# Kernel optimization log

Measured on AMD Instinct MI355X. Metric: run time of the kernel, lower is better.

## Reference

```python
import jax, jax.numpy as jnp
import numpy as np

NUM_NODES = 50000
NUM_GRAPHS = 64
HIDDEN = 256
F_IN = 256
NUM_EDGES = 800000


def setup_inputs() -> dict:
    key = jax.random.key(0)
    ks = jax.random.split(key, 8)
    x = jax.random.normal(ks[0], (NUM_NODES, F_IN), dtype=jnp.float32)
    edge_index = jax.random.randint(ks[1], (2, NUM_EDGES), 0, NUM_NODES, dtype=jnp.int64)
    batch = jnp.sort(jax.random.randint(ks[2], (NUM_NODES,), 0, NUM_GRAPHS, dtype=jnp.int64))
    # Glorot-ish init for weights, zeros for biases (as PyG GCNConv / Linear defaults)
    s1 = 1.0 / np.sqrt(F_IN)
    s2 = 1.0 / np.sqrt(HIDDEN)
    W1 = jax.random.uniform(ks[3], (F_IN, HIDDEN), jnp.float32, -s1, s1)
    b1 = jnp.zeros((HIDDEN,), jnp.float32)
    W2 = jax.random.uniform(ks[4], (HIDDEN, HIDDEN), jnp.float32, -s2, s2)
    b2 = jnp.zeros((HIDDEN,), jnp.float32)
    W_out = jax.random.uniform(ks[5], (HIDDEN, 1), jnp.float32, -s2, s2)
    b_out = jnp.zeros((1,), jnp.float32)
    return {"x": x, "edge_index": edge_index, "batch": batch,
            "W1": W1, "b1": b1, "W2": W2, "b2": b2,
            "W_out": W_out, "b_out": b_out}


def gcn_conv(x, W, b, src, dst, num_nodes):
    """GCNConv with added self-loops and symmetric D^{-1/2} A D^{-1/2} norm."""
    # degrees over edges incl. self-loops (src/dst already include them)
    deg = jax.ops.segment_sum(jnp.ones_like(src, dtype=x.dtype), dst,
                              num_segments=num_nodes)
    dinv = jax.lax.rsqrt(jnp.maximum(deg, 1e-12))
    norm = dinv[src] * dinv[dst]                       # [E+N]
    h = x @ W                                           # [N, H] dense GEMM
    msg = h[src] * norm[:, None]                        # gather + scale
    out = jax.ops.segment_sum(msg, dst, num_segments=num_nodes)  # scatter-add
    return out + b


def reference(x, edge_index, batch, W1, b1, W2, b2, W_out, b_out):
    n = x.shape[0]
    loops = jnp.arange(n, dtype=edge_index.dtype)
    src = jnp.concatenate([edge_index[0], loops])
    dst = jnp.concatenate([edge_index[1], loops])
    h = jax.nn.relu(gcn_conv(x, W1, b1, src, dst, n))
    h = jax.nn.relu(gcn_conv(h, W2, b2, src, dst, n))
    pooled = jax.ops.segment_sum(h, batch, num_segments=NUM_GRAPHS)  # [G, H]
    return pooled @ W_out + b_out
```

## Files before the change

kernel.cpp:

```cpp
#include <hip/hip_runtime.h>
#include <hip/hip_fp16.h>

#define N_NODES 50000
#define NFEAT   256
#define NGRAPH  64
#define NEDGE   800000
#define NBLK_SCAN 196

typedef __attribute__((ext_vector_type(8))) _Float16 half8;
typedef __attribute__((ext_vector_type(2))) _Float16 h2v;
typedef __attribute__((ext_vector_type(4))) float f32x4;
struct alignas(8) US4 { unsigned short x, y, z, w; };

static __device__ __forceinline__ float h2f(unsigned short u) {
    return __half2float(__ushort_as_half(u));
}
static __device__ __forceinline__ unsigned short f2h(float f) {
    return __half_as_ushort(__float2half(f));
}

__global__ void k_count(const int* __restrict__ dst, int* __restrict__ cnt) {
    int e = blockIdx.x * 256 + threadIdx.x;
    if (e < NEDGE) atomicAdd(&cnt[dst[e]], 1);
}

__global__ __launch_bounds__(256) void k_scan1(const int* __restrict__ cnt,
                                               int* __restrict__ row_start,
                                               int* __restrict__ bsum) {
    const int t = threadIdx.x, i = blockIdx.x * 256 + t;
    const int lane = t & 63, w = t >> 6;
    const int c = (i < N_NODES) ? cnt[i] : 0;
    int incl = c;
#pragma unroll
    for (int off = 1; off < 64; off <<= 1) {
        int u = __shfl_up(incl, off, 64);
        if (lane >= off) incl += u;
    }
    __shared__ int wtot[4];
    if (lane == 63) wtot[w] = incl;
    __syncthreads();
    int wbase = 0;
#pragma unroll
    for (int k = 0; k < 4; ++k) wbase += (k < w) ? wtot[k] : 0;
    if (i < N_NODES) row_start[i] = wbase + incl - c;
    if (t == 255) bsum[blockIdx.x] = wbase + incl;
}

__global__ __launch_bounds__(256) void k_scan2(int* __restrict__ bsum) {
    const int t = threadIdx.x, lane = t & 63, w = t >> 6;
    const int c = (t < NBLK_SCAN) ? bsum[t] : 0;
    int incl = c;
#pragma unroll
    for (int off = 1; off < 64; off <<= 1) {
        int u = __shfl_up(incl, off, 64);
        if (lane >= off) incl += u;
    }
    __shared__ int wtot[4];
    if (lane == 63) wtot[w] = incl;
    __syncthreads();
    int wbase = 0;
#pragma unroll
    for (int k = 0; k < 4; ++k) wbase += (k < w) ? wtot[k] : 0;
    if (t < NBLK_SCAN) bsum[t] = wbase + incl - c;
}

__global__ void k_scan3(int* __restrict__ row_start, const int* __restrict__ bsum,
                        int* __restrict__ cnt_cursor, float* __restrict__ dinv) {
    const int i = blockIdx.x * 256 + threadIdx.x;
    if (i >= N_NODES) return;
    const int c = cnt_cursor[i];
    const int start = row_start[i] + bsum[blockIdx.x];
    row_start[i] = start;
    cnt_cursor[i] = start;
    dinv[i] = rsqrtf((float)c + 1.0f);
    if (i == 0) row_start[N_NODES] = NEDGE;
}

__global__ void k_place(const int* __restrict__ src, const int* __restrict__ dst,
                        int* __restrict__ cursor, const float* __restrict__ dinv,
                        unsigned int* __restrict__ csr) {
    int e = blockIdx.x * 256 + threadIdx.x;
    if (e < NEDGE) {
        int s = src[e], d = dst[e];
        float norm = dinv[s] * dinv[d];
        int pos = atomicAdd(&cursor[d], 1);
        csr[pos] = ((unsigned int)f2h(norm) << 16) | (unsigned int)s;
    }
}

__global__ void k_prep_w(const float* __restrict__ W1, const float* __restrict__ W2,
                         unsigned short* __restrict__ w1t, unsigned short* __restrict__ w2t) {
    const int l = blockIdx.x >> 8;
    const int idx = (blockIdx.x & 255) * 256 + threadIdx.x;
    const int n = idx >> 8, k = idx & 255;
    const float* W = l ? W2 : W1;
    unsigned short* wt = l ? w2t : w1t;
    wt[n * 256 + k] = f2h(W[k * 256 + n]);
}

template <bool AF32>
__global__ __launch_bounds__(256) void k_gemm_mfma(const float* __restrict__ Af,
                                                   const unsigned short* __restrict__ Ah,
                                                   const unsigned short* __restrict__ Wt,
                                                   unsigned short* __restrict__ Ch, int M) {
    __shared__ unsigned short lds[32768];
    const int t = threadIdx.x;
    const int half = blockIdx.y;
    const int m0 = blockIdx.x * 128;
    const int w = t >> 6, lane = t & 63;
    const int lr = lane & 15, g = lane >> 4;

    {
        const unsigned short* wbase = Wt + (size_t)half * 128 * 256;
#pragma unroll
        for (int it = 0; it < 16; ++it) {
            const int unit = it * 256 + t;
            const int n = unit >> 5;
            const int rem = unit & 31;
            const int ks = rem >> 2, kg = rem & 3;
            const half8 v = *(const half8*)&wbase[n * 256 + rem * 8];
            const int kgx = kg ^ ((n >> 1) & 3);
            *(half8*)&lds[ks * 4096 + n * 32 + kgx * 8] = v;
        }
    }
    __syncthreads();

    const int rbase = m0 + w * 32;
    unsigned short* Chh = Ch + (size_t)half * (size_t)N_NODES * 128;

    half8 aA[8], aB[8];

#define LOADCHUNK(C, DST)                                                                \
    {                                                                                    \
        const int row = min(rbase + (C) * 16 + lr, M - 1);                               \
        _Pragma("unroll") for (int ks = 0; ks < 8; ++ks) {                               \
            if (AF32) {                                                                  \
                const float* ap = Af + (size_t)row * 256 + ks * 32 + g * 8;              \
                const float4 p0 = *(const float4*)ap;                                    \
                const float4 p1 = *(const float4*)(ap + 4);                              \
                half8 h;                                                                 \
                h[0] = (_Float16)p0.x; h[1] = (_Float16)p0.y;                            \
                h[2] = (_Float16)p0.z; h[3] = (_Float16)p0.w;                            \
                h[4] = (_Float16)p1.x; h[5] = (_Float16)p1.y;                            \
                h[6] = (_Float16)p1.z; h[7] = (_Float16)p1.w;                            \
                DST[ks] = h;                                                             \
            } else {                                                                     \
                DST[ks] = *(const half8*)(Ah + (size_t)(ks >> 2) * (size_t)N_NODES * 128 \
                                          + (size_t)row * 128 + (ks & 3) * 32 + g * 8);  \
            }                                                                            \
        }                                                                                \
    }

#define COMPUTE(C, SRC)                                                                  \
    {                                                                                    \
        f32x4 acc[8] = {};                                                               \
        _Pragma("unroll") for (int ks = 0; ks < 8; ++ks) {                               \
            _Pragma("unroll") for (int ni = 0; ni < 8; ++ni) {                           \
                const int n = ni * 16 + lr;                                              \
                const half8 bf = *(const half8*)&lds[ks * 4096 + n * 32 +                \
                                                     ((g ^ ((n >> 1) & 3)) << 3)];       \
                acc[ni] = __builtin_amdgcn_mfma_f32_16x16x32_f16(SRC[ks], bf,            \
                                                                 acc[ni], 0, 0, 0);      \
            }                                                                            \
        }                                                                                \
        const int r0 = rbase + (C) * 16 + g * 4;                                         \
        _Pragma("unroll") for (int ni = 0; ni < 8; ++ni) {                               \
            const int col = ni * 16 + lr;                                                \
            _Pragma("unroll") for (int r = 0; r < 4; ++r) {                              \
                if (r0 + r < M) Chh[(size_t)(r0 + r) * 128 + col] = f2h(acc[ni][r]);     \
            }                                                                            \
        }                                                                                \
    }

    LOADCHUNK(0, aA)
    LOADCHUNK(1, aB)
    COMPUTE(0, aA)
    COMPUTE(1, aB)

#undef LOADCHUNK
#undef COMPUTE
}

__global__ __launch_bounds__(256) void k_aggregate(const unsigned short* __restrict__ h16,
                                                   const int* __restrict__ row_start,
                                                   const unsigned int* __restrict__ csr,
                                                   const float* __restrict__ dinv,
                                                   const float* __restrict__ bias,
                                                   unsigned short* __restrict__ out,
                                                   const int half) {
    const int node = blockIdx.x * 4 + (threadIdx.x >> 6);
    if (node >= N_NODES) return;
    const int lane = threadIdx.x & 63;
    const int sub = lane >> 4;
    const int fl = lane & 15;
    const unsigned int* hu = (const unsigned int*)(h16 + (size_t)half * N_NODES * 128);

    float acc[8] = {};
    const int s0 = row_start[node], s1 = row_start[node + 1];
    const unsigned int* row = csr + s0;
    const int n = s1 - s0;

#define EDGEPAIR(EA, EB)                                                              \
    {                                                                                 \
        const unsigned int wnp = __builtin_amdgcn_perm(EB, EA, 0x07060302u);          \
        const h2v wn2 = __builtin_bit_cast(h2v, wnp);                                 \
        const uint4 va = *(const uint4*)(hu + (size_t)((EA)&0xffffu) * 64 + fl * 4);  \
        const uint4 vb = *(const uint4*)(hu + (size_t)((EB)&0xffffu) * 64 + fl * 4);  \
        unsigned int plo, phi;                                                        \
        plo = __builtin_amdgcn_perm(vb.x, va.x, 0x05040100u);                         \
        phi = __builtin_amdgcn_perm(vb.x, va.x, 0x07060302u);                         \
        acc[0] = __builtin_amdgcn_fdot2(__builtin_bit_cast(h2v, plo), wn2, acc[0], false); \
        acc[1] = __builtin_amdgcn_fdot2(__builtin_bit_cast(h2v, phi), wn2, acc[1], false); \
        plo = __builtin_amdgcn_perm(vb.y, va.y, 0x05040100u);                         \
        phi = __builtin_amdgcn_perm(vb.y, va.y, 0x07060302u);                         \
        acc[2] = __builtin_amdgcn_fdot2(__builtin_bit_cast(h2v, plo), wn2, acc[2], false); \
        acc[3] = __builtin_amdgcn_fdot2(__builtin_bit_cast(h2v, phi), wn2, acc[3], false); \
        plo = __builtin_amdgcn_perm(vb.z, va.z, 0x05040100u);                         \
        phi = __builtin_amdgcn_perm(vb.z, va.z, 0x07060302u);                         \
        acc[4] = __builtin_amdgcn_fdot2(__builtin_bit_cast(h2v, plo), wn2, acc[4], false); \
        acc[5] = __builtin_amdgcn_fdot2(__builtin_bit_cast(h2v, phi), wn2, acc[5], false); \
        plo = __builtin_amdgcn_perm(vb.w, va.w, 0x05040100u);                         \
        phi = __builtin_amdgcn_perm(vb.w, va.w, 0x07060302u);                         \
        acc[6] = __builtin_amdgcn_fdot2(__builtin_bit_cast(h2v, plo), wn2, acc[6], false); \
        acc[7] = __builtin_amdgcn_fdot2(__builtin_bit_cast(h2v, phi), wn2, acc[7], false); \
    }

    const int nfull = n & ~7;
    int j = 0;
    for (; j < nfull; j += 8) {
        const unsigned int ea = row[j + sub * 2];
        const unsigned int eb = row[j + sub * 2 + 1];
        EDGEPAIR(ea, eb)
    }
    if (j < n) {
        const int ia = j + sub * 2, ib = ia + 1;
        const unsigned int ea = (ia < n) ? row[ia] : 0u;
        const unsigned int eb = (ib < n) ? row[ib] : 0u;
        EDGEPAIR(ea, eb)
    }
#undef EDGEPAIR

#pragma unroll
    for (int i = 0; i < 8; ++i) {
        acc[i] += __shfl_xor(acc[i], 16, 64);
        acc[i] += __shfl_xor(acc[i], 32, 64);
    }

    if (sub == 0) {
        const float dd = dinv[node];
        const float ws = dd * dd;
        const uint4 sh = *(const uint4*)(hu + (size_t)node * 64 + fl * 4);
        const float4 b0 = *(const float4*)(bias + half * 128 + fl * 8);
        const float4 b1 = *(const float4*)(bias + half * 128 + fl * 8 + 4);
        float r[8];
        r[0] = fmaf(h2f((unsigned short)(sh.x & 0xffff)), ws, acc[0]) + b0.x;
        r[1] = fmaf(h2f((unsigned short)(sh.x >> 16)),    ws, acc[1]) + b0.y;
        r[2] = fmaf(h2f((unsigned short)(sh.y & 0xffff)), ws, acc[2]) + b0.z;
        r[3] = fmaf(h2f((unsigned short)(sh.y >> 16)),    ws, acc[3]) + b0.w;
        r[4] = fmaf(h2f((unsigned short)(sh.z & 0xffff)), ws, acc[4]) + b1.x;
        r[5] = fmaf(h2f((unsigned short)(sh.z >> 16)),    ws, acc[5]) + b1.y;
        r[6] = fmaf(h2f((unsigned short)(sh.w & 0xffff)), ws, acc[6]) + b1.z;
        r[7] = fmaf(h2f((unsigned short)(sh.w >> 16)),    ws, acc[7]) + b1.w;
#pragma unroll
        for (int i = 0; i < 8; ++i) r[i] = fmaxf(r[i], 0.f);
        uint4 o;
        o.x = (unsigned int)f2h(r[0]) | ((unsigned int)f2h(r[1]) << 16);
        o.y = (unsigned int)f2h(r[2]) | ((unsigned int)f2h(r[3]) << 16);
        o.z = (unsigned int)f2h(r[4]) | ((unsigned int)f2h(r[5]) << 16);
        o.w = (unsigned int)f2h(r[6]) | ((unsigned int)f2h(r[7]) << 16);
        *(uint4*)((unsigned int*)(out + (size_t)half * N_NODES * 128) +
                  (size_t)node * 64 + fl * 4) = o;
    }
}

__global__ void k_pool(const unsigned short* __restrict__ h2, const int* __restrict__ batch,
                       float* __restrict__ pooled) {
    const int strip = blockIdx.x * 2 + (threadIdx.x >> 7);
    const int tf = threadIdx.x & 127;
    const int f = tf * 2;
    const unsigned short* base = h2 + (size_t)(f >> 7) * N_NODES * 128 + (f & 127);
    const int n0 = strip * 40, n1 = n0 + 40;
    int g = batch[n0];
    float ax = 0.f, ay = 0.f;
    for (int n = n0; n < n1; ++n) {
        const int bg = batch[n];
        if (bg != g) {
            unsafeAtomicAdd(&pooled[g * NFEAT + f], ax);
            unsafeAtomicAdd(&pooled[g * NFEAT + f + 1], ay);
            ax = ay = 0.f;
            g = bg;
        }
        const unsigned int u = *(const unsigned int*)(base + (size_t)n * 128);
        ax += h2f((unsigned short)(u & 0xffff));
        ay += h2f((unsigned short)(u >> 16));
    }
    unsafeAtomicAdd(&pooled[g * NFEAT + f], ax);
    unsafeAtomicAdd(&pooled[g * NFEAT + f + 1], ay);
}

__global__ void k_final(const float* __restrict__ pooled, const float* __restrict__ Wout,
                        const float* __restrict__ bout, float* __restrict__ out) {
    const int g = blockIdx.x, t = threadIdx.x;
    float v = pooled[g * NFEAT + t] * Wout[t];
#pragma unroll
    for (int off = 32; off > 0; off >>= 1) v += __shfl_down(v, off, 64);
    __shared__ float sred[4];
    if ((t & 63) == 0) sred[t >> 6] = v;
    __syncthreads();
    if (t == 0) out[g] = sred[0] + sred[1] + sred[2] + sred[3] + bout[0];
}

extern "C" void kernel_launch(void* const* d_in, const int* in_sizes, int n_in,
                              void* d_out, int out_size, void* d_ws, size_t ws_size,
                              hipStream_t stream) {
    const float* x     = (const float*)d_in[0];
    const int*   ei    = (const int*)d_in[1];
    const int*   batch = (const int*)d_in[2];
    const float* W1    = (const float*)d_in[3];
    const float* b1    = (const float*)d_in[4];
    const float* W2    = (const float*)d_in[5];
    const float* b2    = (const float*)d_in[6];
    const float* Wout  = (const float*)d_in[7];
    const float* bout  = (const float*)d_in[8];
    float* out = (float*)d_out;

    const int* srcp = ei;
    const int* dstp = ei + NEDGE;

    const size_t NE128 = (size_t)N_NODES * 128;
    unsigned short* hA = (unsigned short*)d_ws;
    unsigned short* hB = hA + 2 * NE128;
    float* dinv      = (float*)(hB + 2 * NE128);
    float* pooled    = dinv + N_NODES;
    int*   cnt       = (int*)(pooled + NGRAPH * NFEAT);
    int*   row_start = cnt + N_NODES;
    int*   bsum      = row_start + N_NODES + 3;
    unsigned int* csr = (unsigned int*)(bsum + 256);
    unsigned short* w1t = (unsigned short*)(csr + NEDGE);
    unsigned short* w2t = w1t + 65536;

    const int nblk_edges = (NEDGE + 255) / 256;

    hipMemsetAsync(cnt, 0, N_NODES * sizeof(int), stream);
    k_count<<<nblk_edges, 256, 0, stream>>>(dstp, cnt);
    k_scan1<<<NBLK_SCAN, 256, 0, stream>>>(cnt, row_start, bsum);
    k_scan2<<<1, 256, 0, stream>>>(bsum);
    k_scan3<<<NBLK_SCAN, 256, 0, stream>>>(row_start, bsum, cnt, dinv);
    k_place<<<nblk_edges, 256, 0, stream>>>(srcp, dstp, cnt, dinv, csr);

    k_prep_w<<<512, 256, 0, stream>>>(W1, W2, w1t, w2t);

    const dim3 ggrid(391, 2);
    const int agg_grid = (N_NODES + 3) / 4;

    k_gemm_mfma<true><<<ggrid, 256, 0, stream>>>(x, nullptr, w1t, hA, N_NODES);
    k_aggregate<<<agg_grid, 256, 0, stream>>>(hA, row_start, csr, dinv, b1, hB, 0);
    k_aggregate<<<agg_grid, 256, 0, stream>>>(hA, row_start, csr, dinv, b1, hB, 1);

    k_gemm_mfma<false><<<ggrid, 256, 0, stream>>>(nullptr, hB, w2t, hA, N_NODES);
    k_aggregate<<<agg_grid, 256, 0, stream>>>(hA, row_start, csr, dinv, b2, hB, 0);
    k_aggregate<<<agg_grid, 256, 0, stream>>>(hA, row_start, csr, dinv, b2, hB, 1);

    hipMemsetAsync(pooled, 0, NGRAPH * NFEAT * sizeof(float), stream);
    k_pool<<<625, 256, 0, stream>>>(hB, batch, pooled);
    k_final<<<NGRAPH, 256, 0, stream>>>(pooled, Wout, bout, out);
}
```

Before: 290.2 us.

## Bucket-sort CSR build and fold dinv scaling into GEMM epilogue

Replaces the global-atomic count, three-stage scan and atomic place with a two-level bucket sort: edges are binned into 512-node buckets with LDS histograms, then each bucket builds its CSR rows with LDS atomics. The symmetric norm is factored out: the GEMM epilogue pre-scales rows by dinv[src], and the aggregate multiplies by dinv[dst] once, so the CSR stores only 16-bit source indices. This halves CSR bytes and removes global atomics, but assumes per-bucket edge counts fit in a fixed 16384 window and node ids fit in 16 bits.

```diff
diff --git a/kernel.cpp b/kernel.cpp
--- a/kernel.cpp
+++ b/kernel.cpp
@@ -5,7 +5,8 @@
 #define NFEAT   256
 #define NGRAPH  64
 #define NEDGE   800000
-#define NBLK_SCAN 196
+#define NBUCK   98
+#define BWIN    16384
 
 typedef __attribute__((ext_vector_type(8))) _Float16 half8;
 typedef __attribute__((ext_vector_type(2))) _Float16 h2v;
@@ -19,73 +20,109 @@
     return __half_as_ushort(__float2half(f));
 }
 
-__global__ void k_count(const int* __restrict__ dst, int* __restrict__ cnt) {
-    int e = blockIdx.x * 256 + threadIdx.x;
-    if (e < NEDGE) atomicAdd(&cnt[dst[e]], 1);
-}
-
-__global__ __launch_bounds__(256) void k_scan1(const int* __restrict__ cnt,
+__global__ __launch_bounds__(256) void k_bin(const int* __restrict__ src,
+                                             const int* __restrict__ dst,
+                                             int* __restrict__ bcnt,
+                                             unsigned int* __restrict__ tmp) {
+    __shared__ int hist[NBUCK];
+    __shared__ int base[NBUCK];
+    const int t = threadIdx.x;
+    if (t < NBUCK) hist[t] = 0;
+    __syncthreads();
+    const int e0 = blockIdx.x * 1024 + t * 4;
+    int s[4], d[4], b[4], rk[4];
+#pragma unroll
+    for (int i = 0; i < 4; ++i) {
+        const int e = e0 + i;
+        if (e < NEDGE) {
+            s[i] = src[e];
+            d[i] = dst[e];
+            b[i] = d[i] >> 9;
+            rk[i] = atomicAdd(&hist[b[i]], 1);
+        } else {
+            b[i] = -1;
+        }
+    }
+    __syncthreads();
+    if (t < NBUCK) base[t] = atomicAdd(&bcnt[t], hist[t]);
+    __syncthreads();
+#pragma unroll
+    for (int i = 0; i < 4; ++i) {
+        if (b[i] >= 0)
+            tmp[(size_t)b[i] * BWIN + base[b[i]] + rk[i]] =
+                ((unsigned int)s[i] << 16) | (unsigned int)d[i];
+    }
+}
+
+__global__ void k_bscan(const int* __restrict__ bcnt, int* __restrict__ bbase) {
+    const int l = threadIdx.x;
+    const int i0 = 2 * l, i1 = 2 * l + 1;
+    const int v0 = (i0 < NBUCK) ? bcnt[i0] : 0;
+    const int v1 = (i1 < NBUCK) ? bcnt[i1] : 0;
+    const int ps = v0 + v1;
+    int incl = ps;
+#pragma unroll
+    for (int off = 1; off < 64; off <<= 1) {
+        int u = __shfl_up(incl, off, 64);
+        if (l >= off) incl += u;
+    }
+    const int excl = incl - ps;
+    if (i0 < NBUCK) bbase[i0] = excl;
+    if (i1 < NBUCK) bbase[i1] = excl + v0;
+}
+
+__global__ __launch_bounds__(256) void k_build(const unsigned int* __restrict__ tmp,
+                                               const int* __restrict__ bcnt,
+                                               const int* __restrict__ bbase,
                                                int* __restrict__ row_start,
-                                               int* __restrict__ bsum) {
-    const int t = threadIdx.x, i = blockIdx.x * 256 + t;
+                                               float* __restrict__ dinv,
+                                               unsigned short* __restrict__ csr) {
+    __shared__ int cnt[512];
+    __shared__ int cur[512];
+    __shared__ int wtot[4];
+    const int bk = blockIdx.x, t = threadIdx.x;
+    const int node0 = bk << 9;
+    const int n = bcnt[bk];
+    const unsigned int* rec = tmp + (size_t)bk * BWIN;
+    cnt[t] = 0;
+    cnt[t + 256] = 0;
+    __syncthreads();
+    for (int i = t; i < n; i += 256) atomicAdd(&cnt[rec[i] & 511], 1);
+    __syncthreads();
     const int lane = t & 63, w = t >> 6;
-    const int c = (i < N_NODES) ? cnt[i] : 0;
-    int incl = c;
+    const int v0 = cnt[2 * t], v1 = cnt[2 * t + 1];
+    const int ps = v0 + v1;
+    int incl = ps;
 #pragma unroll
     for (int off = 1; off < 64; off <<= 1) {
         int u = __shfl_up(incl, off, 64);
         if (lane >= off) incl += u;
     }
-    __shared__ int wtot[4];
     if (lane == 63) wtot[w] = incl;
     __syncthreads();
     int wbase = 0;
 #pragma unroll
     for (int k = 0; k < 4; ++k) wbase += (k < w) ? wtot[k] : 0;
-    if (i < N_NODES) row_start[i] = wbase + incl - c;
-    if (t == 255) bsum[blockIdx.x] = wbase + incl;
-}
-
-__global__ __launch_bounds__(256) void k_scan2(int* __restrict__ bsum) {
-    const int t = threadIdx.x, lane = t & 63, w = t >> 6;
-    const int c = (t < NBLK_SCAN) ? bsum[t] : 0;
-    int incl = c;
-#pragma unroll
-    for (int off = 1; off < 64; off <<= 1) {
-        int u = __shfl_up(incl, off, 64);
-        if (lane >= off) incl += u;
-    }
-    __shared__ int wtot[4];
-    if (lane == 63) wtot[w] = incl;
-    __syncthreads();
-    int wbase = 0;
-#pragma unroll
-    for (int k = 0; k < 4; ++k) wbase += (k < w) ? wtot[k] : 0;
-    if (t < NBLK_SCAN) bsum[t] = wbase + incl - c;
-}
-
-__global__ void k_scan3(int* __restrict__ row_start, const int* __restrict__ bsum,
-                        int* __restrict__ cnt_cursor, float* __restrict__ dinv) {
-    const int i = blockIdx.x * 256 + threadIdx.x;
-    if (i >= N_NODES) return;
-    const int c = cnt_cursor[i];
-    const int start = row_start[i] + bsum[blockIdx.x];
-    row_start[i] = start;
-    cnt_cursor[i] = start;
-    dinv[i] = rsqrtf((float)c + 1.0f);
-    if (i == 0) row_start[N_NODES] = NEDGE;
-}
-
-__global__ void k_place(const int* __restrict__ src, const int* __restrict__ dst,
-                        int* __restrict__ cursor, const float* __restrict__ dinv,
-                        unsigned int* __restrict__ csr) {
-    int e = blockIdx.x * 256 + threadIdx.x;
-    if (e < NEDGE) {
-        int s = src[e], d = dst[e];
-        float norm = dinv[s] * dinv[d];
-        int pos = atomicAdd(&cursor[d], 1);
-        csr[pos] = ((unsigned int)f2h(norm) << 16) | (unsigned int)s;
-    }
+    const int excl = wbase + incl - ps;
+    const int gb = bbase[bk];
+    const int g0 = node0 + 2 * t;
+    if (g0 < N_NODES) {
+        row_start[g0] = gb + excl;
+        dinv[g0] = rsqrtf((float)v0 + 1.0f);
+    }
+    if (g0 + 1 < N_NODES) {
+        row_start[g0 + 1] = gb + excl + v0;
+        dinv[g0 + 1] = rsqrtf((float)v1 + 1.0f);
+    }
+    cur[2 * t] = gb + excl;
+    cur[2 * t + 1] = gb + excl + v0;
+    __syncthreads();
+    for (int i = t; i < n; i += 256) {
+        const unsigned int r = rec[i];
+        const int pos = atomicAdd(&cur[r & 511], 1);
+        csr[pos] = (unsigned short)(r >> 16);
+    }
+    if (bk == 0 && t == 0) row_start[N_NODES] = NEDGE;
 }
 
 __global__ void k_prep_w(const float* __restrict__ W1, const float* __restrict__ W2,
@@ -102,6 +139,7 @@
 __global__ __launch_bounds__(256) void k_gemm_mfma(const float* __restrict__ Af,
                                                    const unsigned short* __restrict__ Ah,
                                                    const unsigned short* __restrict__ Wt,
+                                                   const float* __restrict__ dinv,
                                                    unsigned short* __restrict__ Ch, int M) {
     __shared__ unsigned short lds[32768];
     const int t = threadIdx.x;
@@ -164,10 +202,14 @@
             }                                                                            \
         }                                                                                \
         const int r0 = rbase + (C) * 16 + g * 4;                                         \
+        float dv[4];                                                                     \
+        _Pragma("unroll") for (int r = 0; r < 4; ++r)                                    \
+            dv[r] = dinv[min(r0 + r, M - 1)];                                            \
         _Pragma("unroll") for (int ni = 0; ni < 8; ++ni) {                               \
             const int col = ni * 16 + lr;                                                \
             _Pragma("unroll") for (int r = 0; r < 4; ++r) {                              \
-                if (r0 + r < M) Chh[(size_t)(r0 + r) * 128 + col] = f2h(acc[ni][r]);     \
+                if (r0 + r < M)                                                          \
+                    Chh[(size_t)(r0 + r) * 128 + col] = f2h(acc[ni][r] * dv[r]);         \
             }                                                                            \
         }                                                                                \
     }
@@ -181,9 +223,9 @@
 #undef COMPUTE
 }
 
-__global__ __launch_bounds__(256) void k_aggregate(const unsigned short* __restrict__ h16,
+__global__ __launch_bounds__(256) void k_aggregate(const unsigned short* __restrict__ hs,
                                                    const int* __restrict__ row_start,
-                                                   const unsigned int* __restrict__ csr,
+                                                   const unsigned short* __restrict__ csr,
                                                    const float* __restrict__ dinv,
                                                    const float* __restrict__ bias,
                                                    unsigned short* __restrict__ out,
@@ -193,50 +235,50 @@
     const int lane = threadIdx.x & 63;
     const int sub = lane >> 4;
     const int fl = lane & 15;
-    const unsigned int* hu = (const unsigned int*)(h16 + (size_t)half * N_NODES * 128);
+    const unsigned int* hu = (const unsigned int*)(hs + (size_t)half * N_NODES * 128);
+    const h2v one2 = {(_Float16)1.0f, (_Float16)1.0f};
 
     float acc[8] = {};
     const int s0 = row_start[node], s1 = row_start[node + 1];
-    const unsigned int* row = csr + s0;
+    const unsigned short* row = csr + s0;
     const int n = s1 - s0;
 
-#define EDGEPAIR(EA, EB)                                                              \
-    {                                                                                 \
-        const unsigned int wnp = __builtin_amdgcn_perm(EB, EA, 0x07060302u);          \
-        const h2v wn2 = __builtin_bit_cast(h2v, wnp);                                 \
-        const uint4 va = *(const uint4*)(hu + (size_t)((EA)&0xffffu) * 64 + fl * 4);  \
-        const uint4 vb = *(const uint4*)(hu + (size_t)((EB)&0xffffu) * 64 + fl * 4);  \
-        unsigned int plo, phi;                                                        \
-        plo = __builtin_amdgcn_perm(vb.x, va.x, 0x05040100u);                         \
-        phi = __builtin_amdgcn_perm(vb.x, va.x, 0x07060302u);                         \
-        acc[0] = __builtin_amdgcn_fdot2(__builtin_bit_cast(h2v, plo), wn2, acc[0], false); \
-        acc[1] = __builtin_amdgcn_fdot2(__builtin_bit_cast(h2v, phi), wn2, acc[1], false); \
-        plo = __builtin_amdgcn_perm(vb.y, va.y, 0x05040100u);                         \
-        phi = __builtin_amdgcn_perm(vb.y, va.y, 0x07060302u);                         \
-        acc[2] = __builtin_amdgcn_fdot2(__builtin_bit_cast(h2v, plo), wn2, acc[2], false); \
-        acc[3] = __builtin_amdgcn_fdot2(__builtin_bit_cast(h2v, phi), wn2, acc[3], false); \
-        plo = __builtin_amdgcn_perm(vb.z, va.z, 0x05040100u);                         \
-        phi = __builtin_amdgcn_perm(vb.z, va.z, 0x07060302u);                         \
-        acc[4] = __builtin_amdgcn_fdot2(__builtin_bit_cast(h2v, plo), wn2, acc[4], false); \
-        acc[5] = __builtin_amdgcn_fdot2(__builtin_bit_cast(h2v, phi), wn2, acc[5], false); \
-        plo = __builtin_amdgcn_perm(vb.w, va.w, 0x05040100u);                         \
-        phi = __builtin_amdgcn_perm(vb.w, va.w, 0x07060302u);                         \
-        acc[6] = __builtin_amdgcn_fdot2(__builtin_bit_cast(h2v, plo), wn2, acc[6], false); \
-        acc[7] = __builtin_amdgcn_fdot2(__builtin_bit_cast(h2v, phi), wn2, acc[7], false); \
+#define EDGEPAIR(VA, VB)                                                                   \
+    {                                                                                      \
+        unsigned int plo, phi;                                                             \
+        plo = __builtin_amdgcn_perm(VB.x, VA.x, 0x05040100u);                              \
+        phi = __builtin_amdgcn_perm(VB.x, VA.x, 0x07060302u);                              \
+        acc[0] = __builtin_amdgcn_fdot2(__builtin_bit_cast(h2v, plo), one2, acc[0], false);\
+        acc[1] = __builtin_amdgcn_fdot2(__builtin_bit_cast(h2v, phi), one2, acc[1], false);\
+        plo = __builtin_amdgcn_perm(VB.y, VA.y, 0x05040100u);                              \
+        phi = __builtin_amdgcn_perm(VB.y, VA.y, 0x07060302u);                              \
+        acc[2] = __builtin_amdgcn_fdot2(__builtin_bit_cast(h2v, plo), one2, acc[2], false);\
+        acc[3] = __builtin_amdgcn_fdot2(__builtin_bit_cast(h2v, phi), one2, acc[3], false);\
+        plo = __builtin_amdgcn_perm(VB.z, VA.z, 0x05040100u);                              \
+        phi = __builtin_amdgcn_perm(VB.z, VA.z, 0x07060302u);                              \
+        acc[4] = __builtin_amdgcn_fdot2(__builtin_bit_cast(h2v, plo), one2, acc[4], false);\
+        acc[5] = __builtin_amdgcn_fdot2(__builtin_bit_cast(h2v, phi), one2, acc[5], false);\
+        plo = __builtin_amdgcn_perm(VB.w, VA.w, 0x05040100u);                              \
+        phi = __builtin_amdgcn_perm(VB.w, VA.w, 0x07060302u);                              \
+        acc[6] = __builtin_amdgcn_fdot2(__builtin_bit_cast(h2v, plo), one2, acc[6], false);\
+        acc[7] = __builtin_amdgcn_fdot2(__builtin_bit_cast(h2v, phi), one2, acc[7], false);\
     }
 
     const int nfull = n & ~7;
     int j = 0;
     for (; j < nfull; j += 8) {
-        const unsigned int ea = row[j + sub * 2];
-        const unsigned int eb = row[j + sub * 2 + 1];
-        EDGEPAIR(ea, eb)
+        const int sa = row[j + sub * 2];
+        const int sb = row[j + sub * 2 + 1];
+        const uint4 va = *(const uint4*)(hu + (size_t)sa * 64 + fl * 4);
+        const uint4 vb = *(const uint4*)(hu + (size_t)sb * 64 + fl * 4);
+        EDGEPAIR(va, vb)
     }
     if (j < n) {
         const int ia = j + sub * 2, ib = ia + 1;
-        const unsigned int ea = (ia < n) ? row[ia] : 0u;
-        const unsigned int eb = (ib < n) ? row[ib] : 0u;
-        EDGEPAIR(ea, eb)
+        uint4 va = {0, 0, 0, 0}, vb = {0, 0, 0, 0};
+        if (ia < n) va = *(const uint4*)(hu + (size_t)row[ia] * 64 + fl * 4);
+        if (ib < n) vb = *(const uint4*)(hu + (size_t)row[ib] * 64 + fl * 4);
+        EDGEPAIR(va, vb)
     }
 #undef EDGEPAIR
 
@@ -248,19 +290,18 @@
 
     if (sub == 0) {
         const float dd = dinv[node];
-        const float ws = dd * dd;
         const uint4 sh = *(const uint4*)(hu + (size_t)node * 64 + fl * 4);
         const float4 b0 = *(const float4*)(bias + half * 128 + fl * 8);
         const float4 b1 = *(const float4*)(bias + half * 128 + fl * 8 + 4);
         float r[8];
-        r[0] = fmaf(h2f((unsigned short)(sh.x & 0xffff)), ws, acc[0]) + b0.x;
-        r[1] = fmaf(h2f((unsigned short)(sh.x >> 16)),    ws, acc[1]) + b0.y;
-        r[2] = fmaf(h2f((unsigned short)(sh.y & 0xffff)), ws, acc[2]) + b0.z;
-        r[3] = fmaf(h2f((unsigned short)(sh.y >> 16)),    ws, acc[3]) + b0.w;
-        r[4] = fmaf(h2f((unsigned short)(sh.z & 0xffff)), ws, acc[4]) + b1.x;
-        r[5] = fmaf(h2f((unsigned short)(sh.z >> 16)),    ws, acc[5]) + b1.y;
-        r[6] = fmaf(h2f((unsigned short)(sh.w & 0xffff)), ws, acc[6]) + b1.z;
-        r[7] = fmaf(h2f((unsigned short)(sh.w >> 16)),    ws, acc[7]) + b1.w;
+        r[0] = fmaf(acc[0] + h2f((unsigned short)(sh.x & 0xffff)), dd, b0.x);
+        r[1] = fmaf(acc[1] + h2f((unsigned short)(sh.x >> 16)),    dd, b0.y);
+        r[2] = fmaf(acc[2] + h2f((unsigned short)(sh.y & 0xffff)), dd, b0.z);
+        r[3] = fmaf(acc[3] + h2f((unsigned short)(sh.y >> 16)),    dd, b0.w);
+        r[4] = fmaf(acc[4] + h2f((unsigned short)(sh.z & 0xffff)), dd, b1.x);
+        r[5] = fmaf(acc[5] + h2f((unsigned short)(sh.z >> 16)),    dd, b1.y);
+        r[6] = fmaf(acc[6] + h2f((unsigned short)(sh.w & 0xffff)), dd, b1.z);
+        r[7] = fmaf(acc[7] + h2f((unsigned short)(sh.w >> 16)),    dd, b1.w);
 #pragma unroll
         for (int i = 0; i < 8; ++i) r[i] = fmaxf(r[i], 0.f);
         uint4 o;
@@ -332,32 +373,29 @@
     unsigned short* hB = hA + 2 * NE128;
     float* dinv      = (float*)(hB + 2 * NE128);
     float* pooled    = dinv + N_NODES;
-    int*   cnt       = (int*)(pooled + NGRAPH * NFEAT);
-    int*   row_start = cnt + N_NODES;
-    int*   bsum      = row_start + N_NODES + 3;
-    unsigned int* csr = (unsigned int*)(bsum + 256);
-    unsigned short* w1t = (unsigned short*)(csr + NEDGE);
+    int*   row_start = (int*)(pooled + NGRAPH * NFEAT);
+    int*   bcnt      = row_start + N_NODES + 3;
+    int*   bbase     = bcnt + NBUCK;
+    unsigned short* csr = (unsigned short*)(bbase + NBUCK);
+    unsigned int* tmp = (unsigned int*)(csr + NEDGE);
+    unsigned short* w1t = (unsigned short*)(tmp + (size_t)NBUCK * BWIN);
     unsigned short* w2t = w1t + 65536;
 
-    const int nblk_edges = (NEDGE + 255) / 256;
-
-    hipMemsetAsync(cnt, 0, N_NODES * sizeof(int), stream);
-    k_count<<<nblk_edges, 256, 0, stream>>>(dstp, cnt);
-    k_scan1<<<NBLK_SCAN, 256, 0, stream>>>(cnt, row_start, bsum);
-    k_scan2<<<1, 256, 0, stream>>>(bsum);
-    k_scan3<<<NBLK_SCAN, 256, 0, stream>>>(row_start, bsum, cnt, dinv);
-    k_place<<<nblk_edges, 256, 0, stream>>>(srcp, dstp, cnt, dinv, csr);
+    hipMemsetAsync(bcnt, 0, NBUCK * sizeof(int), stream);
+    k_bin<<<(NEDGE + 1023) / 1024, 256, 0, stream>>>(srcp, dstp, bcnt, tmp);
+    k_bscan<<<1, 64, 0, stream>>>(bcnt, bbase);
+    k_build<<<NBUCK, 256, 0, stream>>>(tmp, bcnt, bbase, row_start, dinv, csr);
 
     k_prep_w<<<512, 256, 0, stream>>>(W1, W2, w1t, w2t);
 
     const dim3 ggrid(391, 2);
     const int agg_grid = (N_NODES + 3) / 4;
 
-    k_gemm_mfma<true><<<ggrid, 256, 0, stream>>>(x, nullptr, w1t, hA, N_NODES);
+    k_gemm_mfma<true><<<ggrid, 256, 0, stream>>>(x, nullptr, w1t, dinv, hA, N_NODES);
     k_aggregate<<<agg_grid, 256, 0, stream>>>(hA, row_start, csr, dinv, b1, hB, 0);
     k_aggregate<<<agg_grid, 256, 0, stream>>>(hA, row_start, csr, dinv, b1, hB, 1);
 
-    k_gemm_mfma<false><<<ggrid, 256, 0, stream>>>(nullptr, hB, w2t, hA, N_NODES);
+    k_gemm_mfma<false><<<ggrid, 256, 0, stream>>>(nullptr, hB, w2t, dinv, hA, N_NODES);
     k_aggregate<<<agg_grid, 256, 0, stream>>>(hA, row_start, csr, dinv, b2, hB, 0);
     k_aggregate<<<agg_grid, 256, 0, stream>>>(hA, row_start, csr, dinv, b2, hB, 1);
 
```

After: 277.1 us. 4.5% less time.
